# Kernel tuning notes

Measured on AMD Instinct MI355X. Metric: run time of the kernel, lower is better.

## Reference

```python
import jax, jax.numpy as jnp
import numpy as np

B, N = 65536, 128  # batch of point clouds, points per cloud

def setup_inputs() -> dict:
    key = jax.random.key(0)
    k1, k2 = jax.random.split(key)
    x = jax.random.normal(k1, (B, N, 3), dtype=jnp.float32)
    y = jax.random.normal(k2, (B, N, 3), dtype=jnp.float32)
    return {"x": x, "y": y}

def reference(x, y):
    # zero-center both point clouds
    xc = x - x.mean(axis=-2, keepdims=True)
    yc = y - y.mean(axis=-2, keepdims=True)
    # batched 3x3 covariance: C[..., j, k] = sum_i xc[..., i, j] * yc[..., i, k]
    C = jnp.einsum('...ij,...ik->...jk', xc, yc)
    # torch.linalg.svd returns (U, S, Vh); original code names Vh as V and forms R = U @ Vh
    U, _, Vh = jnp.linalg.svd(C)
    R = jnp.einsum('...ij,...jk->...ik', U, Vh)
    x_aligned = jnp.einsum('...ij,...jk->...ik', xc, R)
    # mean square deviation over all batch, point, and coordinate dims
    return jnp.mean((x_aligned - yc) ** 2)
```

## Files before the change

kernel.cpp:

```cpp
#include <hip/hip_runtime.h>
#include <math.h>


#define NPTS 128
#define WPB 4
#define BLOCKS 512
#define TOTAL_WAVES (BLOCKS * WPB)
#define TILE_F4 192
#define BUF_F4 (2 * TILE_F4)

__device__ __forceinline__ float xsum(float v, int m) {
    return v + __shfl_xor(v, m);
}

__device__ __forceinline__ void stage_tile(const float4* __restrict__ x4,
                                           const float4* __restrict__ y4,
                                           size_t tile, float4* buf, int lane) {
    const size_t base = tile * TILE_F4;
    #pragma unroll
    for (int r = 0; r < 3; ++r) {
        __builtin_amdgcn_global_load_lds(
            (const __attribute__((address_space(1))) void*)(x4 + base + r * 64 + lane),
            (__attribute__((address_space(3))) void*)(buf + r * 64), 16, 0, 0);
        __builtin_amdgcn_global_load_lds(
            (const __attribute__((address_space(1))) void*)(y4 + base + r * 64 + lane),
            (__attribute__((address_space(3))) void*)(buf + TILE_F4 + r * 64), 16, 0, 0);
    }
}

__global__ __launch_bounds__(256, 2) void kabsch_kernel(
        const float4* __restrict__ x4, const float4* __restrict__ y4,
        float* __restrict__ out, float scale, int tilesPerWave) {
    __shared__ float4 smem[WPB][2][BUF_F4];
    __shared__ float wsum[WPB];

    const int tid  = threadIdx.x;
    const int lane = tid & 63;
    const int wave = tid >> 6;
    const int w    = blockIdx.x * WPB + wave;

    float4* buf0 = &smem[wave][0][0];
    float4* buf1 = &smem[wave][1][0];

    stage_tile(x4, y4, (size_t)w, buf0, lane);

    const int g   = lane >> 5;
    const int sub = lane & 31;
    const float invN = 1.0f / (float)NPTS;

    float wave_acc = 0.f;

    for (int t = 0; t < tilesPerWave; ++t) {
        float4* cur = (t & 1) ? buf1 : buf0;
        float4* nxt = (t & 1) ? buf0 : buf1;

        asm volatile("s_waitcnt vmcnt(0)" ::: "memory");

        const float4* xs = cur + g * 96 + sub * 3;
        const float4* ys = cur + TILE_F4 + g * 96 + sub * 3;
        float4 xv0 = xs[0], xv1 = xs[1], xv2 = xs[2];
        float4 yv0 = ys[0], yv1 = ys[1], yv2 = ys[2];

        if (t + 1 < tilesPerWave)
            stage_tile(x4, y4, (size_t)w + (size_t)(t + 1) * TOTAL_WAVES, nxt, lane);

        float fx[12], fy[12];
        fx[0]=xv0.x; fx[1]=xv0.y; fx[2]=xv0.z; fx[3]=xv0.w;
        fx[4]=xv1.x; fx[5]=xv1.y; fx[6]=xv1.z; fx[7]=xv1.w;
        fx[8]=xv2.x; fx[9]=xv2.y; fx[10]=xv2.z; fx[11]=xv2.w;
        fy[0]=yv0.x; fy[1]=yv0.y; fy[2]=yv0.z; fy[3]=yv0.w;
        fy[4]=yv1.x; fy[5]=yv1.y; fy[6]=yv1.z; fy[7]=yv1.w;
        fy[8]=yv2.x; fy[9]=yv2.y; fy[10]=yv2.z; fy[11]=yv2.w;

        float sx0=0.f,sx1=0.f,sx2=0.f, sy0=0.f,sy1=0.f,sy2=0.f;
        float qx=0.f, qy=0.f;
        float c00=0.f,c01=0.f,c02=0.f,c10=0.f,c11=0.f,c12=0.f,
              c20=0.f,c21=0.f,c22=0.f;

        #pragma unroll
        for (int p = 0; p < 4; ++p) {
            float px0=fx[3*p], px1=fx[3*p+1], px2=fx[3*p+2];
            float py0=fy[3*p], py1=fy[3*p+1], py2=fy[3*p+2];
            sx0+=px0; sx1+=px1; sx2+=px2;
            sy0+=py0; sy1+=py1; sy2+=py2;
            qx = fmaf(px0,px0,fmaf(px1,px1,fmaf(px2,px2,qx)));
            qy = fmaf(py0,py0,fmaf(py1,py1,fmaf(py2,py2,qy)));
            c00=fmaf(px0,py0,c00); c01=fmaf(px0,py1,c01); c02=fmaf(px0,py2,c02);
            c10=fmaf(px1,py0,c10); c11=fmaf(px1,py1,c11); c12=fmaf(px1,py2,c12);
            c20=fmaf(px2,py0,c20); c21=fmaf(px2,py1,c21); c22=fmaf(px2,py2,c22);
        }

        #pragma unroll
        for (int m = 1; m <= 16; m <<= 1) {
            sx0=xsum(sx0,m); sx1=xsum(sx1,m); sx2=xsum(sx2,m);
            sy0=xsum(sy0,m); sy1=xsum(sy1,m); sy2=xsum(sy2,m);
            qx =xsum(qx ,m); qy =xsum(qy ,m);
            c00=xsum(c00,m); c01=xsum(c01,m); c02=xsum(c02,m);
            c10=xsum(c10,m); c11=xsum(c11,m); c12=xsum(c12,m);
            c20=xsum(c20,m); c21=xsum(c21,m); c22=xsum(c22,m);
        }

        float C00 = c00 - sx0*sy0*invN, C01 = c01 - sx0*sy1*invN, C02 = c02 - sx0*sy2*invN;
        float C10 = c10 - sx1*sy0*invN, C11 = c11 - sx1*sy1*invN, C12 = c12 - sx1*sy2*invN;
        float C20 = c20 - sx2*sy0*invN, C21 = c21 - sx2*sy1*invN, C22 = c22 - sx2*sy2*invN;
        float Sx = qx - (sx0*sx0 + sx1*sx1 + sx2*sx2) * invN;
        float Sy = qy - (sy0*sy0 + sy1*sy1 + sy2*sy2) * invN;

        float a00 = C00*C00 + C10*C10 + C20*C20;
        float a01 = C00*C01 + C10*C11 + C20*C21;
        float a02 = C00*C02 + C10*C12 + C20*C22;
        float a11 = C01*C01 + C11*C11 + C21*C21;
        float a12 = C01*C02 + C11*C12 + C21*C22;
        float a22 = C02*C02 + C12*C12 + C22*C22;

        float q = (a00 + a11 + a22) * (1.0f / 3.0f);
        float b00 = a00 - q, b11 = a11 - q, b22 = a22 - q;
        float p2 = (b00*b00 + b11*b11 + b22*b22
                    + 2.0f * (a01*a01 + a02*a02 + a12*a12)) * (1.0f / 6.0f);
        float p = sqrtf(fmaxf(p2, 0.0f));
        float detB = b00 * (b11*b22 - a12*a12)
                   - a01 * (a01*b22 - a12*a02)
                   + a02 * (a01*a12 - b11*a02);
        float p3 = p * p * p;
        float r = (p3 > 1e-30f) ? (0.5f * detB / p3) : 0.0f;
        r = fminf(1.0f, fmaxf(-1.0f, r));
        float phi = acosf(r) * (1.0f / 3.0f);
        float two_p = 2.0f * p;
        float l1 = q + two_p * cosf(phi);
        float l3 = q + two_p * cosf(phi + 2.0943951023931953f);
        float l2 = 3.0f * q - l1 - l3;
        float nuc = sqrtf(fmaxf(l1, 0.0f)) + sqrtf(fmaxf(l2, 0.0f))
                  + sqrtf(fmaxf(l3, 0.0f));

        float term = Sx + Sy - 2.0f * nuc;
        term += __shfl_xor(term, 32);
        wave_acc += term;
    }

    if (lane == 0) wsum[wave] = wave_acc;
    __syncthreads();
    if (tid == 0) {
        float tsum = (wsum[0] + wsum[1] + wsum[2] + wsum[3]) * scale;
        atomicAdd(out, tsum);
    }
}

extern "C" void kernel_launch(void* const* d_in, const int* in_sizes, int n_in,
                              void* d_out, int out_size, void* d_ws, size_t ws_size,
                              hipStream_t stream) {
    const float4* x4 = (const float4*)d_in[0];
    const float4* y4 = (const float4*)d_in[1];
    float* out = (float*)d_out;

    const int B = in_sizes[0] / (NPTS * 3);
    const int totalTiles = B / 2;
    const int tilesPerWave = totalTiles / TOTAL_WAVES;
    const float scale = 1.0f / ((float)B * (float)NPTS * 3.0f);

    hipMemsetAsync(out, 0, sizeof(float), stream);
    kabsch_kernel<<<BLOCKS, WPB * 64, 0, stream>>>(x4, y4, out, scale, tilesPerWave);
}
```

Measured before the change: 216.1 us.

## Use DPP reductions, fast intrinsics, merged sums and more blocks

Replaces the shuffle-based 32-lane butterfly reductions with DPP row operations plus row_bcast stages, leaving the final sums in lanes 31 and 63, which are combined with readlane at the end. It merges the x and y sum-of-squares into one accumulator and swaps acosf, cosf, sqrtf and the division for hardware approximations and a polynomial acos. It also raises the grid from 512 to 2048 blocks and the launch-bounds occupancy hint from 2 to 3. The aim is to cut cross-lane shuffle (LDS permute) cost and transcendental instruction count in this compute-bound loop. The approximations lower accuracy, and the p3>1e-30 guard is dropped, so degenerate inputs could produce infinities.

Measured after the change: 216.7 us. No clear change (+0.3%).

```diff
diff --git a/kernel.cpp b/kernel.cpp
--- a/kernel.cpp
+++ b/kernel.cpp
@@ -4,14 +4,10 @@
 
 #define NPTS 128
 #define WPB 4
-#define BLOCKS 512
+#define BLOCKS 2048
 #define TOTAL_WAVES (BLOCKS * WPB)
 #define TILE_F4 192
 #define BUF_F4 (2 * TILE_F4)
-
-__device__ __forceinline__ float xsum(float v, int m) {
-    return v + __shfl_xor(v, m);
-}
 
 __device__ __forceinline__ void stage_tile(const float4* __restrict__ x4,
                                            const float4* __restrict__ y4,
@@ -28,7 +24,24 @@
     }
 }
 
-__global__ __launch_bounds__(256, 2) void kabsch_kernel(
+template<int CTRL, int RMASK>
+__device__ __forceinline__ float dpp_add(float v) {
+    int t = __builtin_amdgcn_update_dpp(0, __builtin_bit_cast(int, v),
+                                        CTRL, RMASK, 0xF, true);
+    return v + __builtin_bit_cast(float, t);
+}
+
+__device__ __forceinline__ float acos_fast(float x) {
+    float ax = fabsf(x);
+    float p = fmaf(ax, -0.0187293f, 0.0742610f);
+    p = fmaf(ax, p, -0.2121144f);
+    p = fmaf(ax, p, 1.5707288f);
+    float s = __builtin_amdgcn_sqrtf(fmaxf(1.0f - ax, 0.0f));
+    float r = s * p;
+    return (x < 0.0f) ? (3.14159265358979f - r) : r;
+}
+
+__global__ __launch_bounds__(256, 3) void kabsch_kernel(
         const float4* __restrict__ x4, const float4* __restrict__ y4,
         float* __restrict__ out, float scale, int tilesPerWave) {
     __shared__ float4 smem[WPB][2][BUF_F4];
@@ -72,8 +85,7 @@
         fy[4]=yv1.x; fy[5]=yv1.y; fy[6]=yv1.z; fy[7]=yv1.w;
         fy[8]=yv2.x; fy[9]=yv2.y; fy[10]=yv2.z; fy[11]=yv2.w;
 
-        float sx0=0.f,sx1=0.f,sx2=0.f, sy0=0.f,sy1=0.f,sy2=0.f;
-        float qx=0.f, qy=0.f;
+        float sx0=0.f,sx1=0.f,sx2=0.f, sy0=0.f,sy1=0.f,sy2=0.f, qq=0.f;
         float c00=0.f,c01=0.f,c02=0.f,c10=0.f,c11=0.f,c12=0.f,
               c20=0.f,c21=0.f,c22=0.f;
 
@@ -83,28 +95,32 @@
             float py0=fy[3*p], py1=fy[3*p+1], py2=fy[3*p+2];
             sx0+=px0; sx1+=px1; sx2+=px2;
             sy0+=py0; sy1+=py1; sy2+=py2;
-            qx = fmaf(px0,px0,fmaf(px1,px1,fmaf(px2,px2,qx)));
-            qy = fmaf(py0,py0,fmaf(py1,py1,fmaf(py2,py2,qy)));
+            qq = fmaf(px0,px0,fmaf(px1,px1,fmaf(px2,px2,qq)));
+            qq = fmaf(py0,py0,fmaf(py1,py1,fmaf(py2,py2,qq)));
             c00=fmaf(px0,py0,c00); c01=fmaf(px0,py1,c01); c02=fmaf(px0,py2,c02);
             c10=fmaf(px1,py0,c10); c11=fmaf(px1,py1,c11); c12=fmaf(px1,py2,c12);
             c20=fmaf(px2,py0,c20); c21=fmaf(px2,py1,c21); c22=fmaf(px2,py2,c22);
         }
 
-        #pragma unroll
-        for (int m = 1; m <= 16; m <<= 1) {
-            sx0=xsum(sx0,m); sx1=xsum(sx1,m); sx2=xsum(sx2,m);
-            sy0=xsum(sy0,m); sy1=xsum(sy1,m); sy2=xsum(sy2,m);
-            qx =xsum(qx ,m); qy =xsum(qy ,m);
-            c00=xsum(c00,m); c01=xsum(c01,m); c02=xsum(c02,m);
-            c10=xsum(c10,m); c11=xsum(c11,m); c12=xsum(c12,m);
-            c20=xsum(c20,m); c21=xsum(c21,m); c22=xsum(c22,m);
-        }
+#define STAGE(C, M) \
+        sx0=dpp_add<C,M>(sx0); sx1=dpp_add<C,M>(sx1); sx2=dpp_add<C,M>(sx2); \
+        sy0=dpp_add<C,M>(sy0); sy1=dpp_add<C,M>(sy1); sy2=dpp_add<C,M>(sy2); \
+        qq =dpp_add<C,M>(qq);                                                \
+        c00=dpp_add<C,M>(c00); c01=dpp_add<C,M>(c01); c02=dpp_add<C,M>(c02); \
+        c10=dpp_add<C,M>(c10); c11=dpp_add<C,M>(c11); c12=dpp_add<C,M>(c12); \
+        c20=dpp_add<C,M>(c20); c21=dpp_add<C,M>(c21); c22=dpp_add<C,M>(c22);
+        STAGE(0xB1, 0xF)
+        STAGE(0x4E, 0xF)
+        STAGE(0x141, 0xF)
+        STAGE(0x140, 0xF)
+        STAGE(0x142, 0xA)
+#undef STAGE
 
         float C00 = c00 - sx0*sy0*invN, C01 = c01 - sx0*sy1*invN, C02 = c02 - sx0*sy2*invN;
         float C10 = c10 - sx1*sy0*invN, C11 = c11 - sx1*sy1*invN, C12 = c12 - sx1*sy2*invN;
         float C20 = c20 - sx2*sy0*invN, C21 = c21 - sx2*sy1*invN, C22 = c22 - sx2*sy2*invN;
-        float Sx = qx - (sx0*sx0 + sx1*sx1 + sx2*sx2) * invN;
-        float Sy = qy - (sy0*sy0 + sy1*sy1 + sy2*sy2) * invN;
+        float Sxy = qq - (sx0*sx0 + sx1*sx1 + sx2*sx2
+                        + sy0*sy0 + sy1*sy1 + sy2*sy2) * invN;
 
         float a00 = C00*C00 + C10*C10 + C20*C20;
         float a01 = C00*C01 + C10*C11 + C20*C21;
@@ -117,27 +133,29 @@
         float b00 = a00 - q, b11 = a11 - q, b22 = a22 - q;
         float p2 = (b00*b00 + b11*b11 + b22*b22
                     + 2.0f * (a01*a01 + a02*a02 + a12*a12)) * (1.0f / 6.0f);
-        float p = sqrtf(fmaxf(p2, 0.0f));
+        float p = __builtin_amdgcn_sqrtf(fmaxf(p2, 0.0f));
         float detB = b00 * (b11*b22 - a12*a12)
                    - a01 * (a01*b22 - a12*a02)
                    + a02 * (a01*a12 - b11*a02);
-        float p3 = p * p * p;
-        float r = (p3 > 1e-30f) ? (0.5f * detB / p3) : 0.0f;
+        float r = 0.5f * detB * __builtin_amdgcn_rcpf(p * p * p);
         r = fminf(1.0f, fmaxf(-1.0f, r));
-        float phi = acosf(r) * (1.0f / 3.0f);
+        float phi_rev = acos_fast(r) * 0.05305164769729845f;
         float two_p = 2.0f * p;
-        float l1 = q + two_p * cosf(phi);
-        float l3 = q + two_p * cosf(phi + 2.0943951023931953f);
+        float l1 = q + two_p * __builtin_amdgcn_cosf(phi_rev);
+        float l3 = q + two_p * __builtin_amdgcn_cosf(phi_rev + 0.33333333333f);
         float l2 = 3.0f * q - l1 - l3;
-        float nuc = sqrtf(fmaxf(l1, 0.0f)) + sqrtf(fmaxf(l2, 0.0f))
-                  + sqrtf(fmaxf(l3, 0.0f));
+        float nuc = __builtin_amdgcn_sqrtf(fmaxf(l1, 0.0f))
+                  + __builtin_amdgcn_sqrtf(fmaxf(l2, 0.0f))
+                  + __builtin_amdgcn_sqrtf(fmaxf(l3, 0.0f));
 
-        float term = Sx + Sy - 2.0f * nuc;
-        term += __shfl_xor(term, 32);
-        wave_acc += term;
+        wave_acc += Sxy - 2.0f * nuc;
     }
 
-    if (lane == 0) wsum[wave] = wave_acc;
+    float t0 = __builtin_bit_cast(float, __builtin_amdgcn_readlane(
+                   __builtin_bit_cast(int, wave_acc), 31));
+    float t1 = __builtin_bit_cast(float, __builtin_amdgcn_readlane(
+                   __builtin_bit_cast(int, wave_acc), 63));
+    if (lane == 0) wsum[wave] = t0 + t1;
     __syncthreads();
     if (tid == 0) {
         float tsum = (wsum[0] + wsum[1] + wsum[2] + wsum[3]) * scale;
```
